# Kernel optimization log

Hardware: AMD Instinct MI355X
Metric: run time of the kernel (lower is better)

The kernel has to match this reference:

```python
import jax, jax.numpy as jnp
import numpy as np

B, L, D, H = 2, 4, 512, 8
HD = D // H
BLOCK, T_IDX, SEM = 2048, 2047, 50
NUM_VQ, CLIP = 1024, 512
T = T_IDX + 1  # condition token + idx tokens


def _ln(x, g, b):
    m = x.mean(-1, keepdims=True)
    v = ((x - m) ** 2).mean(-1, keepdims=True)
    return (x - m) * jax.lax.rsqrt(v + 1e-5) * g + b


def setup_inputs() -> dict:
    key = jax.random.key(0)
    ks = iter(jax.random.split(key, 48))
    p = lambda shape: 0.02 * jax.random.normal(next(ks), shape, jnp.float32)
    inp = {
        'idx': jax.random.randint(next(ks), (B, T_IDX), 0, NUM_VQ + 2, jnp.int32),
        'clip_feature': jax.random.normal(next(ks), (B, CLIP), jnp.float32),
        'tok_emb0': p((NUM_VQ + 2, D)),
        'tok_emb1': p((NUM_VQ + 2, D)),
        'cond_w': p((CLIP, D)), 'cond_b': jnp.zeros((D,), jnp.float32),
        'pos_emb': p((BLOCK, D)),
        'ln1_g': jnp.ones((L, D), jnp.float32), 'ln1_b': jnp.zeros((L, D), jnp.float32),
        'wq': p((L, D, D)), 'bq': jnp.zeros((L, D), jnp.float32),
        'wk': p((L, D, D)), 'bk': jnp.zeros((L, D), jnp.float32),
        'wv': p((L, D, D)), 'bv': jnp.zeros((L, D), jnp.float32),
        'wo': p((L, D, D)), 'bo': jnp.zeros((L, D), jnp.float32),
        'ln2_g': jnp.ones((L, D), jnp.float32), 'ln2_b': jnp.zeros((L, D), jnp.float32),
        'w1': p((L, D, 4 * D)), 'b1': jnp.zeros((L, 4 * D), jnp.float32),
        'w2': p((L, 4 * D, D)), 'b2': jnp.zeros((L, D), jnp.float32),
    }
    return inp


def reference(idx, clip_feature, tok_emb0, tok_emb1, cond_w, cond_b, pos_emb,
              ln1_g, ln1_b, wq, bq, wk, bk, wv, bv, wo, bo,
              ln2_g, ln2_b, w1, b1, w2, b2):
    # condition embedding + dual token embeddings (semantic / reconstruction split)
    cond = (clip_feature @ cond_w + cond_b)[:, None, :]          # [B,1,D]
    sem = tok_emb0[idx[:, :SEM]]                                  # [B,SEM,D]
    rec = tok_emb1[idx[:, SEM:]]                                  # [B,T_IDX-SEM,D]
    x = jnp.concatenate([cond, sem, rec], axis=1) + pos_emb[None, :T]  # [B,T,D]

    scale = 1.0 / np.sqrt(HD)
    causal = jnp.tril(jnp.ones((T, T), bool))                     # key <= query
    for i in range(L):
        h = _ln(x, ln1_g[i], ln1_b[i])
        q = (h @ wq[i] + bq[i]).reshape(B, T, H, HD)
        k = (h @ wk[i] + bk[i]).reshape(B, T, H, HD)
        v = (h @ wv[i] + bv[i]).reshape(B, T, H, HD)
        att = jnp.einsum('bthd,bshd->bhts', q, k) * scale        # [B,H,T,T]
        att = jnp.where(causal, att, -jnp.inf)
        att = jax.nn.softmax(att, axis=-1)
        y = jnp.einsum('bhts,bshd->bthd', att, v).reshape(B, T, D)
        x = x + y @ wo[i] + bo[i]
        h2 = _ln(x, ln2_g[i], ln2_b[i])
        x = x + jax.nn.gelu(h2 @ w1[i] + b1[i], approximate=False) @ w2[i] + b2[i]
    return x
```

## Files before the change

### kernel.cpp

```cpp
#include <hip/hip_runtime.h>
#include <math.h>

#define BB 2
#define TT 2048
#define DD 512
#define LL 4
#define HH 8
#define HDD 64
#define SEMN 50
#define CLIPN 512
#define NTOK (BB*TT)
#define QS 1024
#define VST 2056

typedef __bf16 bf16x8 __attribute__((ext_vector_type(8)));
typedef __bf16 bf16x4 __attribute__((ext_vector_type(4)));
typedef float  f32x4  __attribute__((ext_vector_type(4)));

#if __has_builtin(__builtin_amdgcn_global_load_lds)
#define USE_GLL 1
#endif

__device__ __forceinline__ void gll16(const __bf16* g, __bf16* l) {
#ifdef USE_GLL
  __builtin_amdgcn_global_load_lds((const __attribute__((address_space(1))) void*)g,
                                   (__attribute__((address_space(3))) void*)l, 16, 0, 0);
#endif
}

__device__ __forceinline__ float fexp2(float x) {
#if __has_builtin(__builtin_amdgcn_exp2f)
  return __builtin_amdgcn_exp2f(x);
#else
  return exp2f(x);
#endif
}

__global__ void embed_kernel(const int* __restrict__ idx, const float* __restrict__ clip,
                             const float* __restrict__ tok0, const float* __restrict__ tok1,
                             const float* __restrict__ cw, const float* __restrict__ cb,
                             const float* __restrict__ pos, float* __restrict__ x) {
  int row = blockIdx.x;
  int b = row / TT, t = row % TT;
  int d = threadIdx.x;
  float e;
  if (t == 0) {
    float acc = cb[d];
    for (int c = 0; c < CLIPN; ++c) acc = fmaf(clip[b*CLIPN + c], cw[c*DD + d], acc);
    e = acc;
  } else {
    int tok = idx[b*(TT-1) + (t-1)];
    e = (t <= SEMN) ? tok0[(size_t)tok*DD + d] : tok1[(size_t)tok*DD + d];
  }
  x[(size_t)row*DD + d] = e + pos[(size_t)t*DD + d];
}

__global__ __launch_bounds__(256) void ln_kernel(const float* __restrict__ x,
                                                 const float* __restrict__ g,
                                                 const float* __restrict__ bta,
                                                 __bf16* __restrict__ out) {
  int row = blockIdx.x;
  int tid = threadIdx.x;
  const float* xr = x + (size_t)row * DD;
  float v0 = xr[tid], v1 = xr[tid + 256];
  __shared__ float red[4];
  float s = v0 + v1;
  #pragma unroll
  for (int off = 32; off > 0; off >>= 1) s += __shfl_down(s, off);
  if ((tid & 63) == 0) red[tid >> 6] = s;
  __syncthreads();
  float mean = (red[0] + red[1] + red[2] + red[3]) * (1.0f / DD);
  float d0 = v0 - mean, d1 = v1 - mean;
  float sv = d0*d0 + d1*d1;
  #pragma unroll
  for (int off = 32; off > 0; off >>= 1) sv += __shfl_down(sv, off);
  __syncthreads();
  if ((tid & 63) == 0) red[tid >> 6] = sv;
  __syncthreads();
  float var = (red[0] + red[1] + red[2] + red[3]) * (1.0f / DD);
  float r = rsqrtf(var + 1e-5f);
  out[(size_t)row*DD + tid]       = (__bf16)(d0 * r * g[tid]       + bta[tid]);
  out[(size_t)row*DD + tid + 256] = (__bf16)(d1 * r * g[tid + 256] + bta[tid + 256]);
}

__global__ __launch_bounds__(256) void prep_kernel(
    const float* __restrict__ wq, const float* __restrict__ wk,
    const float* __restrict__ wv, const float* __restrict__ wo,
    const float* __restrict__ w1, const float* __restrict__ w2,
    __bf16* __restrict__ wbuf) {
  __shared__ float tile[32][33];
  int id = blockIdx.x;
  const float* src; __bf16* dst; int K, N, t;
  if (id < 1024) {
    int m = id >> 8; t = id & 255;
    src = (m==0) ? wq : (m==1) ? wk : (m==2) ? wv : wo;
    dst = wbuf + (size_t)m * 262144; K = 512; N = 512;
  } else if (id < 2048) {
    t = id - 1024; src = w1; dst = wbuf + 1048576; K = 512; N = 2048;
  } else {
    t = id - 2048; src = w2; dst = wbuf + 2097152; K = 2048; N = 512;
  }
  int nsh = (N == 2048) ? 6 : 4;
  int tk = t >> nsh, tn = t & ((1 << nsh) - 1);
  int k0 = tk << 5, n0 = tn << 5;
  int tid = threadIdx.x;
  int r = tid >> 3, c = (tid & 7) << 2;
  float4 v = *(const float4*)&src[(size_t)(k0 + r)*N + n0 + c];
  tile[r][c+0] = v.x; tile[r][c+1] = v.y; tile[r][c+2] = v.z; tile[r][c+3] = v.w;
  __syncthreads();
  bf16x4 o;
  o[0] = (__bf16)tile[c+0][r];
  o[1] = (__bf16)tile[c+1][r];
  o[2] = (__bf16)tile[c+2][r];
  o[3] = (__bf16)tile[c+3][r];
  *(bf16x4*)&dst[(size_t)(n0 + r)*K + k0 + c] = o;
}

template<int TM, int TN, int QKV3, int RES, int GEL, int OB>
__global__ __launch_bounds__(256) void mgemm(
    const __bf16* __restrict__ A, const __bf16* __restrict__ Bt,
    const float* __restrict__ b0, const float* __restrict__ b1p, const float* __restrict__ b2p,
    const float* __restrict__ res, float* __restrict__ outF, __bf16* __restrict__ outB,
    __bf16* __restrict__ vtOut, int M, int N, int K, int ldo) {
  __shared__ __bf16 As[TM*32];
  __shared__ __bf16 Bs[TN*32];
  int tid = threadIdx.x, wave = tid >> 6, l = tid & 63;
  int l15 = l & 15, lg = l >> 4;
  int m0 = blockIdx.y * TM, n0 = blockIdx.x * TN;
  constexpr int WR = (TM == 128) ? 2 : 1;
  constexpr int WC = 4 / WR;
  constexpr int FM = TM / (16 * WR);
  constexpr int FN = TN / (16 * WC);
  int wr = wave / WC;
  int wc = wave % WC;

  f32x4 acc[FM][FN] = {};

  for (int k0 = 0; k0 < K; k0 += 32) {
#ifdef USE_GLL
    __syncthreads();
    #pragma unroll
    for (int c = wave; c < TM/16; c += 4) {
      int row = c*16 + (l >> 2);
      int lslot = (l & 3) ^ ((row >> 1) & 3);
      gll16(A + (size_t)(m0+row)*K + k0 + lslot*8, &As[c*512]);
    }
    #pragma unroll
    for (int c = wave; c < TN/16; c += 4) {
      int row = c*16 + (l >> 2);
      int lslot = (l & 3) ^ ((row >> 1) & 3);
      gll16(Bt + (size_t)(n0+row)*K + k0 + lslot*8, &Bs[c*512]);
    }
    asm volatile("s_waitcnt vmcnt(0)" ::: "memory");
    __syncthreads();
#else
    bf16x8 ar[TM/64], br[TN/64];
    #pragma unroll
    for (int c = 0; c < TM/64; ++c) {
      int idx = tid + c*256;
      int row = idx >> 2;
      int lslot = (idx & 3) ^ ((row >> 1) & 3);
      ar[c] = *(const bf16x8*)(A + (size_t)(m0+row)*K + k0 + lslot*8);
    }
    #pragma unroll
    for (int c = 0; c < TN/64; ++c) {
      int idx = tid + c*256;
      int row = idx >> 2;
      int lslot = (idx & 3) ^ ((row >> 1) & 3);
      br[c] = *(const bf16x8*)(Bt + (size_t)(n0+row)*K + k0 + lslot*8);
    }
    __syncthreads();
    #pragma unroll
    for (int c = 0; c < TM/64; ++c) {
      int idx = tid + c*256;
      *(bf16x8*)&As[(idx >> 2)*32 + (idx & 3)*8] = ar[c];
    }
    #pragma unroll
    for (int c = 0; c < TN/64; ++c) {
      int idx = tid + c*256;
      *(bf16x8*)&Bs[(idx >> 2)*32 + (idx & 3)*8] = br[c];
    }
    __syncthreads();
#endif
    bf16x8 af[FM], bfr[FN];
    #pragma unroll
    for (int mi = 0; mi < FM; ++mi) {
      int row = (wr*FM + mi)*16 + l15;
      int ks = lg ^ ((row >> 1) & 3);
      af[mi] = *(const bf16x8*)&As[row*32 + (ks << 3)];
    }
    #pragma unroll
    for (int ni = 0; ni < FN; ++ni) {
      int row = (wc*FN + ni)*16 + l15;
      int ks = lg ^ ((row >> 1) & 3);
      bfr[ni] = *(const bf16x8*)&Bs[row*32 + (ks << 3)];
    }
    #pragma unroll
    for (int mi = 0; mi < FM; ++mi)
      #pragma unroll
      for (int ni = 0; ni < FN; ++ni)
        acc[mi][ni] = __builtin_amdgcn_mfma_f32_16x16x32_bf16(af[mi], bfr[ni], acc[mi][ni], 0, 0, 0);
  }

  #pragma unroll
  for (int mi = 0; mi < FM; ++mi) {
    #pragma unroll
    for (int ni = 0; ni < FN; ++ni) {
      int col = n0 + (wc*FN + ni)*16 + l15;
      float bs;
      if (QKV3) bs = (col < 512) ? b0[col] : (col < 1024) ? b1p[col-512] : b2p[col-1024];
      else bs = b0[col];
      int row0 = m0 + (wr*FM + mi)*16 + (lg << 2);
      if (QKV3 && col >= 1024) {
        int hdg = col - 1024;
        bf16x4 pk;
        #pragma unroll
        for (int r = 0; r < 4; ++r) pk[r] = (__bf16)(acc[mi][ni][r] + bs);
        size_t vrow = (size_t)(((row0 >> 11)*8 + (hdg >> 6))*64 + (hdg & 63));
        *(bf16x4*)&vtOut[vrow*VST + (row0 & 2047)] = pk;
      } else {
        #pragma unroll
        for (int r = 0; r < 4; ++r) {
          int row = row0 + r;
          float v = acc[mi][ni][r] + bs;
          if (RES) v += res[(size_t)row*ldo + col];
          if (GEL) v = 0.5f * v * (1.0f + erff(v * 0.70710678118654752f));
          if (OB) outB[(size_t)row*ldo + col] = (__bf16)v;
          else    outF[(size_t)row*ldo + col] = v;
        }
      }
    }
  }
}

__global__ __launch_bounds__(256) void attn_kernel(const __bf16* __restrict__ qkv,
                                                   const __bf16* __restrict__ vt,
                                                   __bf16* __restrict__ y) {
  __shared__ float po[4][32][68];
  __shared__ float pmS[4][32];
  __shared__ float plS[4][4][32];
  int tid = threadIdx.x, wave = tid >> 6, l = tid & 63;
  int l15 = l & 15, lg = l >> 4;

  int wid = blockIdx.x;
  int g2 = 63 - (wid >> 4);
  int bh = wid & 15;
  int b = bh >> 3, h = bh & 7;
  int q0 = g2 * 32;

  const __bf16* qp = qkv + (size_t)(b*TT)*QS + h*HDD;
  const __bf16* kp = qp + 512;
  const __bf16* vtp = vt + ((size_t)bh*64 + l15)*VST + lg*8;
  const __bf16* kbase = kp + (size_t)l15*QS + lg*8;

  bf16x8 qf[2][2];
  {
    const float qs = 0.125f * 1.44269504088896f;
    #pragma unroll
    for (int f = 0; f < 2; ++f) {
      size_t qr = (size_t)(q0 + f*16 + l15) * QS + lg*8;
      bf16x8 t0 = *(const bf16x8*)(qp + qr);
      bf16x8 t1 = *(const bf16x8*)(qp + qr + 32);
      #pragma unroll
      for (int e = 0; e < 8; ++e) {
        qf[f][0][e] = (__bf16)((float)t0[e] * qs);
        qf[f][1][e] = (__bf16)((float)t1[e] * qs);
      }
    }
  }

  f32x4 o[2][4] = {};
  float m0 = 0.f, m1 = 0.f, ls0 = 0.f, ls1 = 0.f;
  int qpos0 = q0 + l15, qpos1 = q0 + 16 + l15;
  int nt = (q0 + 95) >> 6;
  int cs = (nt + 3) >> 2;
  int t0w = wave * cs;
  int t1w = t0w + cs; if (t1w > nt) t1w = nt;

  bf16x8 kA[4][2], kB[4][2], vv[8];

#define KLOAD(DST, KT) do {                                         \
    const __bf16* kr_ = kbase + (size_t)(KT)*64*QS;                 \
    _Pragma("unroll")                                               \
    for (int j_ = 0; j_ < 4; ++j_) {                                \
      DST[j_][0] = *(const bf16x8*)(kr_ + j_*16*QS);                \
      DST[j_][1] = *(const bf16x8*)(kr_ + j_*16*QS + 32);           \
    }                                                               \
  } while (0)

#define VLOAD(KT) do {                                              \
    const __bf16* vr_ = vtp + (KT)*64;                              \
    _Pragma("unroll")                                               \
    for (int hc_ = 0; hc_ < 4; ++hc_) {                             \
      vv[hc_]     = *(const bf16x8*)(vr_ + hc_*16*VST);             \
      vv[hc_ + 4] = *(const bf16x8*)(vr_ + hc_*16*VST + 32);        \
    }                                                               \
  } while (0)

#define PROCESS(KF, KT) do {                                                             \
    float sv[2][4][4];                                                                   \
    _Pragma("unroll")                                                                    \
    for (int f = 0; f < 2; ++f)                                                          \
      _Pragma("unroll")                                                                  \
      for (int j = 0; j < 4; ++j) {                                                      \
        f32x4 a_ = {};                                                                   \
        a_ = __builtin_amdgcn_mfma_f32_16x16x32_bf16(KF[j][0], qf[f][0], a_, 0, 0, 0);   \
        a_ = __builtin_amdgcn_mfma_f32_16x16x32_bf16(KF[j][1], qf[f][1], a_, 0, 0, 0);   \
        _Pragma("unroll")                                                                \
        for (int r = 0; r < 4; ++r) sv[f][j][r] = a_[r];                                 \
      }                                                                                  \
    if ((KT) == nt - 1) {                                                                \
      _Pragma("unroll")                                                                  \
      for (int j = 0; j < 4; ++j) {                                                      \
        int kb0 = (KT)*64 + j*16 + lg*4;                                                 \
        _Pragma("unroll")                                                                \
        for (int r = 0; r < 4; ++r) {                                                    \
          if (kb0 + r > qpos0) sv[0][j][r] = -1e30f;                                     \
          if (kb0 + r > qpos1) sv[1][j][r] = -1e30f;                                     \
        }                                                                                \
      }                                                                                  \
    }                                                                                    \
    float px0 = sv[0][0][0], px1 = sv[1][0][0];                                          \
    _Pragma("unroll")                                                                    \
    for (int j = 0; j < 4; ++j)                                                          \
      _Pragma("unroll")                                                                  \
      for (int r = 0; r < 4; ++r) {                                                      \
        px0 = fmaxf(px0, sv[0][j][r]);                                                   \
        px1 = fmaxf(px1, sv[1][j][r]);                                                   \
      }                                                                                  \
    if (!__all((px0 - m0 <= 8.0f) && (px1 - m1 <= 8.0f))) {                              \
      float u0 = px0, w0 = px0, u1 = px1, w1 = px1;                                      \
      asm("v_permlane32_swap_b32 %0, %1" : "+v"(u0), "+v"(w0));                          \
      float t0_ = fmaxf(u0, w0); u0 = t0_; w0 = t0_;                                     \
      asm("v_permlane16_swap_b32 %0, %1" : "+v"(u0), "+v"(w0));                          \
      float tm0 = fmaxf(u0, w0);                                                         \
      asm("v_permlane32_swap_b32 %0, %1" : "+v"(u1), "+v"(w1));                          \
      float t1_ = fmaxf(u1, w1); u1 = t1_; w1 = t1_;                                     \
      asm("v_permlane16_swap_b32 %0, %1" : "+v"(u1), "+v"(w1));                          \
      float tm1 = fmaxf(u1, w1);                                                         \
      float mn0 = fmaxf(m0, tm0), mn1 = fmaxf(m1, tm1);                                  \
      float fc0 = fexp2(m0 - mn0), fc1 = fexp2(m1 - mn1);                                \
      m0 = mn0; m1 = mn1;                                                                \
      ls0 *= fc0; ls1 *= fc1;                                                            \
      float a0_ = __shfl(fc0, lg*4+0), a1_ = __shfl(fc0, lg*4+1);                        \
      float a2_ = __shfl(fc0, lg*4+2), a3_ = __shfl(fc0, lg*4+3);                        \
      float b0_ = __shfl(fc1, lg*4+0), b1_ = __shfl(fc1, lg*4+1);                        \
      float b2_ = __shfl(fc1, lg*4+2), b3_ = __shfl(fc1, lg*4+3);                        \
      _Pragma("unroll")                                                                  \
      for (int hc = 0; hc < 4; ++hc) {                                                   \
        o[0][hc][0] *= a0_; o[0][hc][1] *= a1_; o[0][hc][2] *= a2_; o[0][hc][3] *= a3_;  \
        o[1][hc][0] *= b0_; o[1][hc][1] *= b1_; o[1][hc][2] *= b2_; o[1][hc][3] *= b3_;  \
      }                                                                                  \
    }                                                                                    \
    _Pragma("unroll")                                                                    \
    for (int f = 0; f < 2; ++f) {                                                        \
      float mm = f ? m1 : m0;                                                            \
      float p_[4][4];                                                                    \
      float rs_ = 0.f;                                                                   \
      _Pragma("unroll")                                                                  \
      for (int j = 0; j < 4; ++j)                                                        \
        _Pragma("unroll")                                                                \
        for (int r = 0; r < 4; ++r) { p_[j][r] = fexp2(sv[f][j][r] - mm); rs_ += p_[j][r]; } \
      if (f) ls1 += rs_; else ls0 += rs_;                                                \
      union PU { unsigned u[4]; bf16x8 v; };                                             \
      PU pa0, pa1;                                                                       \
      _Pragma("unroll")                                                                  \
      for (int pair = 0; pair < 2; ++pair) {                                             \
        unsigned c0, c1, d0, d1;                                                         \
        asm("v_cvt_pk_bf16_f32 %0, %1, %2" : "=v"(c0) : "v"(p_[2*pair][0]),   "v"(p_[2*pair][1]));   \
        asm("v_cvt_pk_bf16_f32 %0, %1, %2" : "=v"(c1) : "v"(p_[2*pair][2]),   "v"(p_[2*pair][3]));   \
        asm("v_cvt_pk_bf16_f32 %0, %1, %2" : "=v"(d0) : "v"(p_[2*pair+1][0]), "v"(p_[2*pair+1][1])); \
        asm("v_cvt_pk_bf16_f32 %0, %1, %2" : "=v"(d1) : "v"(p_[2*pair+1][2]), "v"(p_[2*pair+1][3])); \
        asm("v_permlane32_swap_b32 %0, %1" : "+v"(c0), "+v"(d0));                        \
        asm("v_permlane32_swap_b32 %0, %1" : "+v"(c1), "+v"(d1));                        \
        asm("v_permlane16_swap_b32 %0, %1" : "+v"(c0), "+v"(d0));                        \
        asm("v_permlane16_swap_b32 %0, %1" : "+v"(c1), "+v"(d1));                        \
        PU& pa = pair ? pa1 : pa0;                                                       \
        pa.u[0] = c0; pa.u[1] = c1; pa.u[2] = d0; pa.u[3] = d1;                          \
      }                                                                                  \
      _Pragma("unroll")                                                                  \
      for (int hc = 0; hc < 4; ++hc) {                                                   \
        o[f][hc] = __builtin_amdgcn_mfma_f32_16x16x32_bf16(pa0.v, vv[hc],     o[f][hc], 0, 0, 0); \
        o[f][hc] = __builtin_amdgcn_mfma_f32_16x16x32_bf16(pa1.v, vv[hc + 4], o[f][hc], 0, 0, 0); \
      }                                                                                  \
    }                                                                                    \
  } while (0)

  if (t0w < t1w) {
    KLOAD(kA, t0w);
    int kt = t0w;
    while (true) {
      VLOAD(kt);
      if (kt + 1 < t1w) KLOAD(kB, kt + 1);
      PROCESS(kA, kt);
      ++kt; if (kt >= t1w) break;
      VLOAD(kt);
      if (kt + 1 < t1w) KLOAD(kA, kt + 1);
      PROCESS(kB, kt);
      ++kt; if (kt >= t1w) break;
    }
  }

  #pragma unroll
  for (int f = 0; f < 2; ++f)
    #pragma unroll
    for (int hc = 0; hc < 4; ++hc)
      #pragma unroll
      for (int r = 0; r < 4; ++r)
        po[wave][f*16 + lg*4 + r][hc*16 + l15] = o[f][hc][r];
  plS[wave][lg][l15]      = ls0;
  plS[wave][lg][16 + l15] = ls1;
  if (l < 16) { pmS[wave][l] = m0; pmS[wave][16 + l] = m1; }
  __syncthreads();

  #pragma unroll
  for (int rep = 0; rep < 2; ++rep) {
    int q = wave*4 + lg + rep*16;
    float e0 = pmS[0][q], e1 = pmS[1][q], e2 = pmS[2][q], e3 = pmS[3][q];
    float mstar = fmaxf(fmaxf(e0, e1), fmaxf(e2, e3));
    float f0 = fexp2(e0 - mstar), f1 = fexp2(e1 - mstar);
    float f2 = fexp2(e2 - mstar), f3 = fexp2(e3 - mstar);
    float l0 = plS[0][0][q] + plS[0][1][q] + plS[0][2][q] + plS[0][3][q];
    float l1 = plS[1][0][q] + plS[1][1][q] + plS[1][2][q] + plS[1][3][q];
    float l2 = plS[2][0][q] + plS[2][1][q] + plS[2][2][q] + plS[2][3][q];
    float l3 = plS[3][0][q] + plS[3][1][q] + plS[3][2][q] + plS[3][3][q];
    float lstar = l0*f0 + l1*f1 + l2*f2 + l3*f3;
    float inv = 1.0f / lstar;
    f32x4 o0 = *(const f32x4*)&po[0][q][l15*4];
    f32x4 o1 = *(const f32x4*)&po[1][q][l15*4];
    f32x4 o2 = *(const f32x4*)&po[2][q][l15*4];
    f32x4 o3 = *(const f32x4*)&po[3][q][l15*4];
    bf16x4 outv;
    #pragma unroll
    for (int j = 0; j < 4; ++j)
      outv[j] = (__bf16)((o0[j]*f0 + o1[j]*f1 + o2[j]*f2 + o3[j]*f3) * inv);
    size_t base = (size_t)(b*TT + q0 + q) * DD + h*HDD + l15*4;
    *(bf16x4*)&y[base] = outv;
  }
}

extern "C" void kernel_launch(void* const* d_in, const int* in_sizes, int n_in,
                              void* d_out, int out_size, void* d_ws, size_t ws_size,
                              hipStream_t stream) {
  const int*   idx    = (const int*)d_in[0];
  const float* clip   = (const float*)d_in[1];
  const float* tok0   = (const float*)d_in[2];
  const float* tok1   = (const float*)d_in[3];
  const float* cond_w = (const float*)d_in[4];
  const float* cond_b = (const float*)d_in[5];
  const float* pos    = (const float*)d_in[6];
  const float* ln1_g  = (const float*)d_in[7];
  const float* ln1_b  = (const float*)d_in[8];
  const float* wq     = (const float*)d_in[9];
  const float* bq     = (const float*)d_in[10];
  const float* wk     = (const float*)d_in[11];
  const float* bk     = (const float*)d_in[12];
  const float* wv     = (const float*)d_in[13];
  const float* bv     = (const float*)d_in[14];
  const float* wo     = (const float*)d_in[15];
  const float* bo     = (const float*)d_in[16];
  const float* ln2_g  = (const float*)d_in[17];
  const float* ln2_b  = (const float*)d_in[18];
  const float* w1     = (const float*)d_in[19];
  const float* b1     = (const float*)d_in[20];
  const float* w2     = (const float*)d_in[21];
  const float* b2     = (const float*)d_in[22];

  float* x = (float*)d_out;
  char* wsb = (char*)d_ws;
  __bf16* wbuf = (__bf16*)wsb;
  __bf16* h    = (__bf16*)(wsb + 6291456);
  __bf16* qkv  = (__bf16*)(wsb + 10485760);
  __bf16* yb   = (__bf16*)(wsb + 23068672);
  __bf16* ffn  = qkv;
  __bf16* vt   = (__bf16*)(wsb + 27262976);

  embed_kernel<<<dim3(NTOK), 512, 0, stream>>>(idx, clip, tok0, tok1, cond_w, cond_b, pos, x);

  for (int i = 0; i < LL; ++i) {
    prep_kernel<<<dim3(3072), 256, 0, stream>>>(
        wq + (size_t)i*262144, wk + (size_t)i*262144, wv + (size_t)i*262144,
        wo + (size_t)i*262144, w1 + (size_t)i*1048576, w2 + (size_t)i*1048576, wbuf);

    ln_kernel<<<NTOK, 256, 0, stream>>>(x, ln1_g + i*DD, ln1_b + i*DD, h);

    mgemm<64,128,1,0,0,1><<<dim3(12, 64), 256, 0, stream>>>(
        h, wbuf, bq + i*DD, bk + i*DD, bv + i*DD, nullptr, nullptr, qkv, vt, NTOK, 1536, 512, 1024);

    attn_kernel<<<dim3(1024), 256, 0, stream>>>(qkv, vt, yb);

    mgemm<64,64,0,1,0,0><<<dim3(8, 64), 256, 0, stream>>>(
        yb, wbuf + 786432, bo + i*DD, nullptr, nullptr, x, x, nullptr, nullptr, NTOK, 512, 512, 512);

    ln_kernel<<<NTOK, 256, 0, stream>>>(x, ln2_g + i*DD, ln2_b + i*DD, h);

    mgemm<64,128,0,0,1,1><<<dim3(16, 64), 256, 0, stream>>>(
        h, wbuf + 1048576, b1 + (size_t)i*4*DD, nullptr, nullptr, nullptr, nullptr, ffn, nullptr, NTOK, 4*DD, 512, 2048);

    mgemm<64,64,0,1,0,0><<<dim3(8, 64), 256, 0, stream>>>(
        ffn, wbuf + 2097152, b2 + i*DD, nullptr, nullptr, x, x, nullptr, nullptr, NTOK, 512, 2048, 512);
  }
}
```

Measured before the change: 529.9 us.

## Batch weight prep across layers, vectorize embed and layernorm, enlarge FFN1 tile

Converts all four layers' weights to bf16 in a single launch when the workspace is large enough, replacing four per-layer prep launches. LayerNorm now handles one row per wavefront with 8-wide vector loads and xor shuffles, with no shared-memory barriers. The embed kernel uses float4 accesses. The first FFN GEMM moves to a 128x128 tile. Costs are more workspace, a fallback path that depends on workspace size, and fewer blocks for the FFN GEMM.

```diff
diff --git a/kernel.cpp b/kernel.cpp
--- a/kernel.cpp
+++ b/kernel.cpp
@@ -36,69 +36,83 @@
 #endif
 }
 
-__global__ void embed_kernel(const int* __restrict__ idx, const float* __restrict__ clip,
-                             const float* __restrict__ tok0, const float* __restrict__ tok1,
-                             const float* __restrict__ cw, const float* __restrict__ cb,
-                             const float* __restrict__ pos, float* __restrict__ x) {
+__global__ __launch_bounds__(128) void embed_kernel(
+    const int* __restrict__ idx, const float* __restrict__ clip,
+    const float* __restrict__ tok0, const float* __restrict__ tok1,
+    const float* __restrict__ cw, const float* __restrict__ cb,
+    const float* __restrict__ pos, float* __restrict__ x) {
   int row = blockIdx.x;
   int b = row / TT, t = row % TT;
-  int d = threadIdx.x;
-  float e;
+  int d4 = threadIdx.x << 2;
+  float4 e;
   if (t == 0) {
-    float acc = cb[d];
-    for (int c = 0; c < CLIPN; ++c) acc = fmaf(clip[b*CLIPN + c], cw[c*DD + d], acc);
+    float4 acc = *(const float4*)&cb[d4];
+    const float* cr = clip + b*CLIPN;
+    for (int c = 0; c < CLIPN; ++c) {
+      float cv = cr[c];
+      float4 w4 = *(const float4*)&cw[(size_t)c*DD + d4];
+      acc.x = fmaf(cv, w4.x, acc.x); acc.y = fmaf(cv, w4.y, acc.y);
+      acc.z = fmaf(cv, w4.z, acc.z); acc.w = fmaf(cv, w4.w, acc.w);
+    }
     e = acc;
   } else {
     int tok = idx[b*(TT-1) + (t-1)];
-    e = (t <= SEMN) ? tok0[(size_t)tok*DD + d] : tok1[(size_t)tok*DD + d];
-  }
-  x[(size_t)row*DD + d] = e + pos[(size_t)t*DD + d];
+    const float* te = (t <= SEMN) ? tok0 : tok1;
+    e = *(const float4*)&te[(size_t)tok*DD + d4];
+  }
+  float4 p = *(const float4*)&pos[(size_t)t*DD + d4];
+  e.x += p.x; e.y += p.y; e.z += p.z; e.w += p.w;
+  *(float4*)&x[(size_t)row*DD + d4] = e;
 }
 
 __global__ __launch_bounds__(256) void ln_kernel(const float* __restrict__ x,
                                                  const float* __restrict__ g,
                                                  const float* __restrict__ bta,
                                                  __bf16* __restrict__ out) {
-  int row = blockIdx.x;
-  int tid = threadIdx.x;
-  const float* xr = x + (size_t)row * DD;
-  float v0 = xr[tid], v1 = xr[tid + 256];
-  __shared__ float red[4];
-  float s = v0 + v1;
+  int l = threadIdx.x & 63;
+  int row = blockIdx.x * 4 + (threadIdx.x >> 6);
+  const float* xr = x + (size_t)row * DD + l*8;
+  f32x4 a = *(const f32x4*)xr;
+  f32x4 c = *(const f32x4*)(xr + 4);
+  float s = a[0]+a[1]+a[2]+a[3]+c[0]+c[1]+c[2]+c[3];
   #pragma unroll
-  for (int off = 32; off > 0; off >>= 1) s += __shfl_down(s, off);
-  if ((tid & 63) == 0) red[tid >> 6] = s;
-  __syncthreads();
-  float mean = (red[0] + red[1] + red[2] + red[3]) * (1.0f / DD);
-  float d0 = v0 - mean, d1 = v1 - mean;
-  float sv = d0*d0 + d1*d1;
+  for (int off = 1; off < 64; off <<= 1) s += __shfl_xor(s, off);
+  float mean = s * (1.0f / DD);
+  float d0 = a[0]-mean, d1 = a[1]-mean, d2 = a[2]-mean, d3 = a[3]-mean;
+  float d4 = c[0]-mean, d5 = c[1]-mean, d6 = c[2]-mean, d7 = c[3]-mean;
+  float sv = d0*d0+d1*d1+d2*d2+d3*d3+d4*d4+d5*d5+d6*d6+d7*d7;
   #pragma unroll
-  for (int off = 32; off > 0; off >>= 1) sv += __shfl_down(sv, off);
-  __syncthreads();
-  if ((tid & 63) == 0) red[tid >> 6] = sv;
-  __syncthreads();
-  float var = (red[0] + red[1] + red[2] + red[3]) * (1.0f / DD);
-  float r = rsqrtf(var + 1e-5f);
-  out[(size_t)row*DD + tid]       = (__bf16)(d0 * r * g[tid]       + bta[tid]);
-  out[(size_t)row*DD + tid + 256] = (__bf16)(d1 * r * g[tid + 256] + bta[tid + 256]);
+  for (int off = 1; off < 64; off <<= 1) sv += __shfl_xor(sv, off);
+  float r = rsqrtf(sv * (1.0f / DD) + 1e-5f);
+  f32x4 gv0 = *(const f32x4*)&g[l*8],   gv1 = *(const f32x4*)&g[l*8+4];
+  f32x4 bv0 = *(const f32x4*)&bta[l*8], bv1 = *(const f32x4*)&bta[l*8+4];
+  bf16x8 o;
+  o[0] = (__bf16)(d0*r*gv0[0] + bv0[0]); o[1] = (__bf16)(d1*r*gv0[1] + bv0[1]);
+  o[2] = (__bf16)(d2*r*gv0[2] + bv0[2]); o[3] = (__bf16)(d3*r*gv0[3] + bv0[3]);
+  o[4] = (__bf16)(d4*r*gv1[0] + bv1[0]); o[5] = (__bf16)(d5*r*gv1[1] + bv1[1]);
+  o[6] = (__bf16)(d6*r*gv1[2] + bv1[2]); o[7] = (__bf16)(d7*r*gv1[3] + bv1[3]);
+  *(bf16x8*)&out[(size_t)row*DD + l*8] = o;
 }
 
 __global__ __launch_bounds__(256) void prep_kernel(
     const float* __restrict__ wq, const float* __restrict__ wk,
     const float* __restrict__ wv, const float* __restrict__ wo,
     const float* __restrict__ w1, const float* __restrict__ w2,
-    __bf16* __restrict__ wbuf) {
+    __bf16* __restrict__ wbuf, size_t dstride) {
   __shared__ float tile[32][33];
   int id = blockIdx.x;
+  int lay = blockIdx.y;
+  size_t so4 = (size_t)lay * 262144, so16 = (size_t)lay * 1048576;
+  __bf16* wb = wbuf + (size_t)lay * dstride;
   const float* src; __bf16* dst; int K, N, t;
   if (id < 1024) {
     int m = id >> 8; t = id & 255;
-    src = (m==0) ? wq : (m==1) ? wk : (m==2) ? wv : wo;
-    dst = wbuf + (size_t)m * 262144; K = 512; N = 512;
+    src = ((m==0) ? wq : (m==1) ? wk : (m==2) ? wv : wo) + so4;
+    dst = wb + (size_t)m * 262144; K = 512; N = 512;
   } else if (id < 2048) {
-    t = id - 1024; src = w1; dst = wbuf + 1048576; K = 512; N = 2048;
+    t = id - 1024; src = w1 + so16; dst = wb + 1048576; K = 512; N = 2048;
   } else {
-    t = id - 2048; src = w2; dst = wbuf + 2097152; K = 2048; N = 512;
+    t = id - 2048; src = w2 + so16; dst = wb + 2097152; K = 2048; N = 512;
   }
   int nsh = (N == 2048) ? 6 : 4;
   int tk = t >> nsh, tn = t & ((1 << nsh) - 1);
@@ -468,36 +482,56 @@
 
   float* x = (float*)d_out;
   char* wsb = (char*)d_ws;
-  __bf16* wbuf = (__bf16*)wsb;
-  __bf16* h    = (__bf16*)(wsb + 6291456);
-  __bf16* qkv  = (__bf16*)(wsb + 10485760);
-  __bf16* yb   = (__bf16*)(wsb + 23068672);
-  __bf16* ffn  = qkv;
-  __bf16* vt   = (__bf16*)(wsb + 27262976);
-
-  embed_kernel<<<dim3(NTOK), 512, 0, stream>>>(idx, clip, tok0, tok1, cond_w, cond_b, pos, x);
+  bool bigws = ws_size >= 46153728ULL;
+
+  __bf16* wbuf; __bf16* h; __bf16* qkv; __bf16* yb; __bf16* vt; __bf16* ffn;
+  size_t wstride;
+  if (bigws) {
+    wbuf = (__bf16*)wsb;
+    wstride = 3145728;
+    h    = (__bf16*)(wsb + 25165824);
+    qkv  = (__bf16*)(wsb + 29360128);
+    yb   = (__bf16*)(wsb + 37748736);
+    vt   = (__bf16*)(wsb + 41943040);
+    ffn  = qkv;
+  } else {
+    wbuf = (__bf16*)wsb;
+    wstride = 0;
+    h    = (__bf16*)(wsb + 6291456);
+    qkv  = (__bf16*)(wsb + 10485760);
+    yb   = (__bf16*)(wsb + 23068672);
+    vt   = (__bf16*)(wsb + 27262976);
+    ffn  = qkv;
+  }
+
+  embed_kernel<<<dim3(NTOK), 128, 0, stream>>>(idx, clip, tok0, tok1, cond_w, cond_b, pos, x);
+
+  if (bigws)
+    prep_kernel<<<dim3(3072, LL), 256, 0, stream>>>(wq, wk, wv, wo, w1, w2, wbuf, wstride);
 
   for (int i = 0; i < LL; ++i) {
-    prep_kernel<<<dim3(3072), 256, 0, stream>>>(
-        wq + (size_t)i*262144, wk + (size_t)i*262144, wv + (size_t)i*262144,
-        wo + (size_t)i*262144, w1 + (size_t)i*1048576, w2 + (size_t)i*1048576, wbuf);
-
-    ln_kernel<<<NTOK, 256, 0, stream>>>(x, ln1_g + i*DD, ln1_b + i*DD, h);
+    __bf16* wb = wbuf + (size_t)i * wstride;
+    if (!bigws)
+      prep_kernel<<<dim3(3072, 1), 256, 0, stream>>>(
+          wq + (size_t)i*262144, wk + (size_t)i*262144, wv + (size_t)i*262144,
+          wo + (size_t)i*262144, w1 + (size_t)i*1048576, w2 + (size_t)i*1048576, wb, 0);
+
+    ln_kernel<<<NTOK/4, 256, 0, stream>>>(x, ln1_g + i*DD, ln1_b + i*DD, h);
 
     mgemm<64,128,1,0,0,1><<<dim3(12, 64), 256, 0, stream>>>(
-        h, wbuf, bq + i*DD, bk + i*DD, bv + i*DD, nullptr, nullptr, qkv, vt, NTOK, 1536, 512, 1024);
+        h, wb, bq + i*DD, bk + i*DD, bv + i*DD, nullptr, nullptr, qkv, vt, NTOK, 1536, 512, 1024);
 
     attn_kernel<<<dim3(1024), 256, 0, stream>>>(qkv, vt, yb);
 
     mgemm<64,64,0,1,0,0><<<dim3(8, 64), 256, 0, stream>>>(
-        yb, wbuf + 786432, bo + i*DD, nullptr, nullptr, x, x, nullptr, nullptr, NTOK, 512, 512, 512);
-
-    ln_kernel<<<NTOK, 256, 0, stream>>>(x, ln2_g + i*DD, ln2_b + i*DD, h);
-
-    mgemm<64,128,0,0,1,1><<<dim3(16, 64), 256, 0, stream>>>(
-        h, wbuf + 1048576, b1 + (size_t)i*4*DD, nullptr, nullptr, nullptr, nullptr, ffn, nullptr, NTOK, 4*DD, 512, 2048);
+        yb, wb + 786432, bo + i*DD, nullptr, nullptr, x, x, nullptr, nullptr, NTOK, 512, 512, 512);
+
+    ln_kernel<<<NTOK/4, 256, 0, stream>>>(x, ln2_g + i*DD, ln2_b + i*DD, h);
+
+    mgemm<128,128,0,0,1,1><<<dim3(16, 32), 256, 0, stream>>>(
+        h, wb + 1048576, b1 + (size_t)i*4*DD, nullptr, nullptr, nullptr, nullptr, ffn, nullptr, NTOK, 4*DD, 512, 2048);
 
     mgemm<64,64,0,1,0,0><<<dim3(8, 64), 256, 0, stream>>>(
-        ffn, wbuf + 2097152, b2 + i*DD, nullptr, nullptr, x, x, nullptr, nullptr, NTOK, 512, 2048, 512);
-  }
-}
+        ffn, wb + 2097152, b2 + i*DD, nullptr, nullptr, x, x, nullptr, nullptr, NTOK, 512, 2048, 512);
+  }
+}
```

Measured after the change: 519.7 us. No clear change (-1.9%).
